# Optimization experiments

Measured on AMD Instinct MI355X. Metric: run time of the kernel, lower is better.

The kernel has to match this reference:

```python
import jax, jax.numpy as jnp
import numpy as np

NEG = -1000000.0

def setup_inputs() -> dict:
    key = jax.random.key(0)
    k1, k2, k3, k4, k5 = jax.random.split(key, 5)
    B, Lq, Lm, Din, Dout = 8, 2048, 2048, 1024, 1024
    query = jax.random.normal(k1, (B, Lq, Din), dtype=jnp.float32)
    memories = jax.random.normal(k2, (B, Lm, Dout), dtype=jnp.float32)
    mask = jax.random.randint(k3, (B, Lq, Lm), 0, 2, dtype=jnp.int32)
    # Linear(in_features=1024, out_features=1024)
    bound = 1.0 / np.sqrt(Din)
    W = jax.random.uniform(k4, (Dout, Din), minval=-bound, maxval=bound, dtype=jnp.float32)
    b = jax.random.uniform(k5, (Dout,), minval=-bound, maxval=bound, dtype=jnp.float32)
    return {"query": query, "memories": memories, "mask": mask, "W": W, "b": b}

def reference(query, memories, mask, W, b):
    # projected query: [B, Lq, Dout]
    q = jnp.einsum('bqi,oi->bqo', query, W) + b
    # additive binary mask: 1 -> 0, 0 -> -1e6
    add_mask = (1.0 - mask.astype(q.dtype)) * NEG
    # unscaled Luong scores: [B, Lq, Lm]
    logits = jnp.einsum('bqd,bmd->bqm', q, memories) + add_mask
    weights = jax.nn.softmax(logits, axis=-1)
    out = jnp.einsum('bqm,bmd->bqd', weights, memories)
    return out
```

## Files before the change

kernel.cpp:

```cpp
#include <hip/hip_runtime.h>

typedef float    f32x4 __attribute__((ext_vector_type(4)));
typedef _Float16 f16x4 __attribute__((ext_vector_type(4)));
typedef _Float16 f16x8 __attribute__((ext_vector_type(8)));

__device__ __forceinline__ void gload16(const void* g, void* l) {
  __builtin_amdgcn_global_load_lds(
      (const __attribute__((address_space(1))) void*)g,
      (__attribute__((address_space(3))) void*)l, 16, 0, 0);
}

#define MFMA16(d, a, b) __builtin_amdgcn_mfma_f32_16x16x32_f16(a, b, d, 0, 0, 0)

template <bool STG>
__device__ __forceinline__ void ktile256(
    char* L, int d, size_t go,
    const char* aSrc0, const char* aSrc1,
    const char* bSrc0, const char* bSrc1,
    int ldsStage, int wr, int wc, int l15, int rcb,
    f32x4 (&acc)[8][4]) {
  const char* Ab0 = L + d * 32768;
  const char* Bb0 = L + 65536 + d * 32768;
  const int dn = d ^ 1;
  f16x8 af[8], bf[2];

  #pragma unroll
  for (int m = 0; m < 8; m++)
    af[m] = *(const f16x8*)(Ab0 + (wr + m * 16 + l15) * 64 + rcb);
  #pragma unroll
  for (int n = 0; n < 2; n++)
    bf[n] = *(const f16x8*)(Bb0 + (wc + n * 16 + l15) * 64 + rcb);
  if constexpr (STG) {
    char* dst = L + dn * 32768 + ldsStage;
    gload16(aSrc0 + go, dst);
    gload16(aSrc1 + go, dst + 1024);
  }
  __builtin_amdgcn_s_barrier();
  __builtin_amdgcn_s_setprio(1);
  #pragma unroll
  for (int m = 0; m < 8; m++) {
    acc[m][0] = MFMA16(acc[m][0], af[m], bf[0]);
    acc[m][1] = MFMA16(acc[m][1], af[m], bf[1]);
  }
  __builtin_amdgcn_s_setprio(0);
  __builtin_amdgcn_s_barrier();

  #pragma unroll
  for (int n = 0; n < 2; n++)
    bf[n] = *(const f16x8*)(Bb0 + (wc + (2 + n) * 16 + l15) * 64 + rcb);
  if constexpr (STG) {
    char* dst = L + 65536 + dn * 32768 + ldsStage;
    gload16(bSrc0 + go, dst);
    gload16(bSrc1 + go, dst + 1024);
    asm volatile("s_waitcnt vmcnt(4)" ::: "memory");
  } else {
    asm volatile("s_waitcnt vmcnt(0)" ::: "memory");
  }
  __builtin_amdgcn_s_barrier();
  __builtin_amdgcn_s_setprio(1);
  #pragma unroll
  for (int m = 0; m < 8; m++) {
    acc[m][2] = MFMA16(acc[m][2], af[m], bf[0]);
    acc[m][3] = MFMA16(acc[m][3], af[m], bf[1]);
  }
  __builtin_amdgcn_s_setprio(0);
  __builtin_amdgcn_s_barrier();

  #pragma unroll
  for (int m = 0; m < 8; m++)
    af[m] = *(const f16x8*)(Ab0 + 16384 + (wr + m * 16 + l15) * 64 + rcb);
  #pragma unroll
  for (int n = 0; n < 2; n++)
    bf[n] = *(const f16x8*)(Bb0 + 16384 + (wc + n * 16 + l15) * 64 + rcb);
  if constexpr (STG) {
    char* dst = L + dn * 32768 + 16384 + ldsStage;
    gload16(aSrc0 + go + 64, dst);
    gload16(aSrc1 + go + 64, dst + 1024);
  }
  __builtin_amdgcn_s_barrier();
  __builtin_amdgcn_s_setprio(1);
  #pragma unroll
  for (int m = 0; m < 8; m++) {
    acc[m][0] = MFMA16(acc[m][0], af[m], bf[0]);
    acc[m][1] = MFMA16(acc[m][1], af[m], bf[1]);
  }
  __builtin_amdgcn_s_setprio(0);
  __builtin_amdgcn_s_barrier();

  #pragma unroll
  for (int n = 0; n < 2; n++)
    bf[n] = *(const f16x8*)(Bb0 + 16384 + (wc + (2 + n) * 16 + l15) * 64 + rcb);
  if constexpr (STG) {
    char* dst = L + 65536 + dn * 32768 + 16384 + ldsStage;
    gload16(bSrc0 + go + 64, dst);
    gload16(bSrc1 + go + 64, dst + 1024);
    asm volatile("s_waitcnt vmcnt(4)" ::: "memory");
  }
  __builtin_amdgcn_s_barrier();
  __builtin_amdgcn_s_setprio(1);
  #pragma unroll
  for (int m = 0; m < 8; m++) {
    acc[m][2] = MFMA16(acc[m][2], af[m], bf[0]);
    acc[m][3] = MFMA16(acc[m][3], af[m], bf[1]);
  }
  __builtin_amdgcn_s_setprio(0);
  __builtin_amdgcn_s_barrier();
}

template <typename TOUT, bool BIAS>
__global__ __launch_bounds__(512) void gemm256(
    const _Float16* __restrict__ A, const _Float16* __restrict__ B,
    const float* __restrict__ bias, TOUT* __restrict__ Cp,
    int M, int N, int K, long sA, long sB, long sC) {
  __shared__ _Float16 lds[65536];
  char* const L = (char*)lds;
  const int tid = threadIdx.x;
  const int w = tid >> 6, l = tid & 63;
  const int l15 = l & 15, q = l >> 4;
  const int wr = (w >> 2) * 128, wc = (w & 3) * 64;
  const int m0 = blockIdx.y * 256, n0 = blockIdx.x * 256;
  const _Float16* Ab = A + (size_t)blockIdx.z * sA;
  const _Float16* Bb = B + (size_t)blockIdx.z * sB;

  const int scb = ((l & 3) ^ q) << 4;
  const int sr0 = w * 32 + (l >> 2);
  const char* aSrc0 = (const char*)(Ab + (size_t)(m0 + sr0) * K) + scb;
  const char* aSrc1 = (const char*)(Ab + (size_t)(m0 + sr0 + 16) * K) + scb;
  const char* bSrc0 = (const char*)(Bb + (size_t)(n0 + sr0) * K) + scb;
  const char* bSrc1 = (const char*)(Bb + (size_t)(n0 + sr0 + 16) * K) + scb;
  const int ldsStage = w * 2048;
  const int rcb = ((q ^ (l15 >> 2)) << 4);

  f32x4 acc[8][4] = {};
  const int NT = K >> 6;

  {
    char* dA = L + ldsStage;
    char* dB = L + 65536 + ldsStage;
    gload16(aSrc0, dA);       gload16(aSrc1, dA + 1024);
    gload16(bSrc0, dB);       gload16(bSrc1, dB + 1024);
    gload16(aSrc0 + 64, dA + 16384); gload16(aSrc1 + 64, dA + 16384 + 1024);
    gload16(bSrc0 + 64, dB + 16384); gload16(bSrc1 + 64, dB + 16384 + 1024);
    asm volatile("s_waitcnt vmcnt(4)" ::: "memory");
  }
  __builtin_amdgcn_s_barrier();

  for (int t = 0; t < NT - 1; ++t)
    ktile256<true>(L, t & 1, (size_t)(t + 1) * 128, aSrc0, aSrc1, bSrc0, bSrc1,
                   ldsStage, wr, wc, l15, rcb, acc);
  ktile256<false>(L, (NT - 1) & 1, 0, aSrc0, aSrc1, bSrc0, bSrc1,
                  ldsStage, wr, wc, l15, rcb, acc);

  TOUT* C = Cp + (size_t)blockIdx.z * sC;
  const int q4 = q * 4;
  #pragma unroll
  for (int n = 0; n < 4; n++) {
    int col = n0 + wc + n * 16 + l15;
    float bb = BIAS ? bias[col] : 0.0f;
    #pragma unroll
    for (int m = 0; m < 8; m++) {
      int rowb = m0 + wr + m * 16 + q4;
      #pragma unroll
      for (int rr = 0; rr < 4; rr++)
        C[(size_t)(rowb + rr) * N + col] = (TOUT)(acc[m][n][rr] + bb);
    }
  }
}

__global__ __launch_bounds__(256) void transpose16_kernel(
    const _Float16* __restrict__ src, _Float16* __restrict__ dst) {
  const int Lm = 2048, D = 1024;
  __shared__ _Float16 tile[64 * 64];
  const int d0 = blockIdx.x * 64, m0 = blockIdx.y * 64;
  const _Float16* s = src + (size_t)blockIdx.z * Lm * D;
  _Float16*       d = dst + (size_t)blockIdx.z * D * Lm;
  const int tid = threadIdx.x;
  #pragma unroll
  for (int it = 0; it < 2; it++) {
    int idx = tid + it * 256;
    int mm = idx >> 3, g = idx & 7;
    int pg = g ^ ((mm >> 3) & 7);
    *(f16x8*)&tile[mm * 64 + pg * 8] =
        *(const f16x8*)&s[(size_t)(m0 + mm) * D + d0 + g * 8];
  }
  __syncthreads();
  #pragma unroll
  for (int it = 0; it < 2; it++) {
    int idx = tid + it * 256;
    int dd = idx >> 3, mc = (idx & 7) * 8;
    f16x8 h;
    #pragma unroll
    for (int j = 0; j < 8; j++) {
      int row = mc + j;
      int pg = (dd >> 3) ^ ((row >> 3) & 7);
      h[j] = tile[row * 64 + pg * 8 + (dd & 7)];
    }
    *(f16x8*)&d[(size_t)(d0 + dd) * Lm + m0 + mc] = h;
  }
}

__global__ __launch_bounds__(256) void softmax_kernel(
    const int* __restrict__ mask, _Float16* __restrict__ wbuf) {
  const int Lm = 2048;
  size_t row = blockIdx.x;
  _Float16* wr = wbuf + row * Lm;
  const int* mr = mask + row * Lm;
  int tid = threadIdx.x;
  f16x8 lv = *(const f16x8*)&wr[tid * 8];
  int4 ma = *(const int4*)&mr[tid * 8];
  int4 mb = *(const int4*)&mr[tid * 8 + 4];
  int mk[8] = {ma.x, ma.y, ma.z, ma.w, mb.x, mb.y, mb.z, mb.w};
  float v[8];
  float mx = -3.0e38f;
  #pragma unroll
  for (int i = 0; i < 8; i++) {
    float l = (float)lv[i];
    if (mk[i] == 0) l += -1000000.0f;
    v[i] = l;
    mx = fmaxf(mx, l);
  }
  #pragma unroll
  for (int off = 32; off > 0; off >>= 1) mx = fmaxf(mx, __shfl_down(mx, off, 64));
  __shared__ float red[4];
  int wv = tid >> 6;
  if ((tid & 63) == 0) red[wv] = mx;
  __syncthreads();
  mx = fmaxf(fmaxf(red[0], red[1]), fmaxf(red[2], red[3]));
  __syncthreads();
  float s = 0.f;
  #pragma unroll
  for (int i = 0; i < 8; i++) { v[i] = __expf(v[i] - mx); s += v[i]; }
  #pragma unroll
  for (int off = 32; off > 0; off >>= 1) s += __shfl_down(s, off, 64);
  if ((tid & 63) == 0) red[wv] = s;
  __syncthreads();
  float inv = 1.0f / (red[0] + red[1] + red[2] + red[3]);
  f16x8 o;
  #pragma unroll
  for (int i = 0; i < 8; i++) o[i] = (_Float16)(v[i] * inv);
  *(f16x8*)&wr[tid * 8] = o;
}

__global__ __launch_bounds__(256) void cvt8_kernel(const float* __restrict__ x,
                                                   _Float16* __restrict__ y) {
  size_t i = (size_t)(blockIdx.x * 256 + threadIdx.x) * 8;
  f32x4 a = *(const f32x4*)&x[i];
  f32x4 b = *(const f32x4*)&x[i + 4];
  f16x8 h = {(_Float16)a[0], (_Float16)a[1], (_Float16)a[2], (_Float16)a[3],
             (_Float16)b[0], (_Float16)b[1], (_Float16)b[2], (_Float16)b[3]};
  *(f16x8*)&y[i] = h;
}

extern "C" void kernel_launch(void* const* d_in, const int* in_sizes, int n_in,
                              void* d_out, int out_size, void* d_ws, size_t ws_size,
                              hipStream_t stream) {
  const float* query = (const float*)d_in[0];
  const float* mem   = (const float*)d_in[1];
  const int*   mask  = (const int*)d_in[2];
  const float* W     = (const float*)d_in[3];
  const float* bias  = (const float*)d_in[4];
  float* out = (float*)d_out;

  char* ws = (char*)d_ws;
  _Float16* qproj  = (_Float16*)ws;
  _Float16* memT   = (_Float16*)ws;
  _Float16* queryh = (_Float16*)(ws + (size_t)32 * 1024 * 1024);
  _Float16* Wh     = (_Float16*)(ws + (size_t)64 * 1024 * 1024);
  _Float16* wbuf   = (_Float16*)(ws + (size_t)32 * 1024 * 1024);
  _Float16* memh   = (_Float16*)d_out;

  const long LQK = 2048L * 1024, LQM = 2048L * 2048;

  cvt8_kernel<<<dim3(512),  256, 0, stream>>>(W, Wh);
  cvt8_kernel<<<dim3(8192), 256, 0, stream>>>(query, queryh);
  cvt8_kernel<<<dim3(8192), 256, 0, stream>>>(mem, memh);
  gemm256<_Float16, true><<<dim3(4, 64, 1), 512, 0, stream>>>(
      queryh, Wh, bias, qproj, 16384, 1024, 1024, 0, 0, 0);
  gemm256<_Float16, false><<<dim3(8, 8, 8), 512, 0, stream>>>(
      qproj, memh, nullptr, wbuf, 2048, 2048, 1024, LQK, LQK, LQM);
  softmax_kernel<<<dim3(16384), 256, 0, stream>>>(mask, wbuf);
  transpose16_kernel<<<dim3(16, 32, 8), 256, 0, stream>>>(memh, memT);
  gemm256<float, false><<<dim3(4, 8, 8), 512, 0, stream>>>(
      wbuf, memT, nullptr, out, 2048, 1024, 2048, LQM, LQK, LQK);
}
```

Baseline: 514.2 us.

## Reorder MFMA phases to 4x4 sub-tiles and change LDS swizzle pattern

```diff
diff --git a/kernel.cpp b/kernel.cpp
--- a/kernel.cpp
+++ b/kernel.cpp
@@ -22,13 +22,13 @@
   const char* Ab0 = L + d * 32768;
   const char* Bb0 = L + 65536 + d * 32768;
   const int dn = d ^ 1;
-  f16x8 af[8], bf[2];
-
-  #pragma unroll
-  for (int m = 0; m < 8; m++)
+  f16x8 af[4], bf[4];
+
+  #pragma unroll
+  for (int m = 0; m < 4; m++)
     af[m] = *(const f16x8*)(Ab0 + (wr + m * 16 + l15) * 64 + rcb);
   #pragma unroll
-  for (int n = 0; n < 2; n++)
+  for (int n = 0; n < 4; n++)
     bf[n] = *(const f16x8*)(Bb0 + (wc + n * 16 + l15) * 64 + rcb);
   if constexpr (STG) {
     char* dst = L + dn * 32768 + ldsStage;
@@ -38,16 +38,16 @@
   __builtin_amdgcn_s_barrier();
   __builtin_amdgcn_s_setprio(1);
   #pragma unroll
-  for (int m = 0; m < 8; m++) {
-    acc[m][0] = MFMA16(acc[m][0], af[m], bf[0]);
-    acc[m][1] = MFMA16(acc[m][1], af[m], bf[1]);
-  }
-  __builtin_amdgcn_s_setprio(0);
-  __builtin_amdgcn_s_barrier();
-
-  #pragma unroll
-  for (int n = 0; n < 2; n++)
-    bf[n] = *(const f16x8*)(Bb0 + (wc + (2 + n) * 16 + l15) * 64 + rcb);
+  for (int m = 0; m < 4; m++)
+    #pragma unroll
+    for (int n = 0; n < 4; n++)
+      acc[m][n] = MFMA16(acc[m][n], af[m], bf[n]);
+  __builtin_amdgcn_s_setprio(0);
+  __builtin_amdgcn_s_barrier();
+
+  #pragma unroll
+  for (int m = 0; m < 4; m++)
+    af[m] = *(const f16x8*)(Ab0 + (wr + (4 + m) * 16 + l15) * 64 + rcb);
   if constexpr (STG) {
     char* dst = L + 65536 + dn * 32768 + ldsStage;
     gload16(bSrc0 + go, dst);
@@ -59,18 +59,18 @@
   __builtin_amdgcn_s_barrier();
   __builtin_amdgcn_s_setprio(1);
   #pragma unroll
-  for (int m = 0; m < 8; m++) {
-    acc[m][2] = MFMA16(acc[m][2], af[m], bf[0]);
-    acc[m][3] = MFMA16(acc[m][3], af[m], bf[1]);
-  }
-  __builtin_amdgcn_s_setprio(0);
-  __builtin_amdgcn_s_barrier();
-
-  #pragma unroll
-  for (int m = 0; m < 8; m++)
+  for (int m = 0; m < 4; m++)
+    #pragma unroll
+    for (int n = 0; n < 4; n++)
+      acc[4 + m][n] = MFMA16(acc[4 + m][n], af[m], bf[n]);
+  __builtin_amdgcn_s_setprio(0);
+  __builtin_amdgcn_s_barrier();
+
+  #pragma unroll
+  for (int m = 0; m < 4; m++)
     af[m] = *(const f16x8*)(Ab0 + 16384 + (wr + m * 16 + l15) * 64 + rcb);
   #pragma unroll
-  for (int n = 0; n < 2; n++)
+  for (int n = 0; n < 4; n++)
     bf[n] = *(const f16x8*)(Bb0 + 16384 + (wc + n * 16 + l15) * 64 + rcb);
   if constexpr (STG) {
     char* dst = L + dn * 32768 + 16384 + ldsStage;
@@ -80,16 +80,16 @@
   __builtin_amdgcn_s_barrier();
   __builtin_amdgcn_s_setprio(1);
   #pragma unroll
-  for (int m = 0; m < 8; m++) {
-    acc[m][0] = MFMA16(acc[m][0], af[m], bf[0]);
-    acc[m][1] = MFMA16(acc[m][1], af[m], bf[1]);
-  }
-  __builtin_amdgcn_s_setprio(0);
-  __builtin_amdgcn_s_barrier();
-
-  #pragma unroll
-  for (int n = 0; n < 2; n++)
-    bf[n] = *(const f16x8*)(Bb0 + 16384 + (wc + (2 + n) * 16 + l15) * 64 + rcb);
+  for (int m = 0; m < 4; m++)
+    #pragma unroll
+    for (int n = 0; n < 4; n++)
+      acc[m][n] = MFMA16(acc[m][n], af[m], bf[n]);
+  __builtin_amdgcn_s_setprio(0);
+  __builtin_amdgcn_s_barrier();
+
+  #pragma unroll
+  for (int m = 0; m < 4; m++)
+    af[m] = *(const f16x8*)(Ab0 + 16384 + (wr + (4 + m) * 16 + l15) * 64 + rcb);
   if constexpr (STG) {
     char* dst = L + 65536 + dn * 32768 + 16384 + ldsStage;
     gload16(bSrc0 + go + 64, dst);
@@ -99,10 +99,10 @@
   __builtin_amdgcn_s_barrier();
   __builtin_amdgcn_s_setprio(1);
   #pragma unroll
-  for (int m = 0; m < 8; m++) {
-    acc[m][2] = MFMA16(acc[m][2], af[m], bf[0]);
-    acc[m][3] = MFMA16(acc[m][3], af[m], bf[1]);
-  }
+  for (int m = 0; m < 4; m++)
+    #pragma unroll
+    for (int n = 0; n < 4; n++)
+      acc[4 + m][n] = MFMA16(acc[4 + m][n], af[m], bf[n]);
   __builtin_amdgcn_s_setprio(0);
   __builtin_amdgcn_s_barrier();
 }
@@ -122,14 +122,14 @@
   const _Float16* Ab = A + (size_t)blockIdx.z * sA;
   const _Float16* Bb = B + (size_t)blockIdx.z * sB;
 
-  const int scb = ((l & 3) ^ q) << 4;
+  const int scb = (((l & 3) ^ ((l >> 3) & 3)) << 4);
   const int sr0 = w * 32 + (l >> 2);
   const char* aSrc0 = (const char*)(Ab + (size_t)(m0 + sr0) * K) + scb;
   const char* aSrc1 = (const char*)(Ab + (size_t)(m0 + sr0 + 16) * K) + scb;
   const char* bSrc0 = (const char*)(Bb + (size_t)(n0 + sr0) * K) + scb;
   const char* bSrc1 = (const char*)(Bb + (size_t)(n0 + sr0 + 16) * K) + scb;
   const int ldsStage = w * 2048;
-  const int rcb = ((q ^ (l15 >> 2)) << 4);
+  const int rcb = ((q ^ ((l15 >> 1) & 3)) << 4);
 
   f32x4 acc[8][4] = {};
   const int NT = K >> 6;
```

Result: no change. 508.8 us (-1.0%).
